# Kernel optimization log

Measured on AMD Instinct MI355X. Metric: run time of the kernel, lower is better.

## Reference

```python
import jax, jax.numpy as jnp
import numpy as np

SCALING = 32.0 / 16.0  # lora_alpha / r

HIDDEN = 4096
FFN = 14336
R = 16
TOKENS = 4096


def _lora(x, A, a_b, B, b_b):
    # nn.Linear: y = x @ W.T + b ; EVELinear: (B(A(x))) * scaling
    h = x @ A.T + a_b            # [tokens, r]
    return (h @ B.T + b_b) * SCALING  # [tokens, out]


def setup_inputs() -> dict:
    key = jax.random.key(0)
    ks = jax.random.split(key, 13)
    s = 0.02
    inp = {
        "x": jax.random.normal(ks[0], (TOKENS, HIDDEN), dtype=jnp.float32),
        # w1: hidden -> ffn
        "w1_A": jax.random.normal(ks[1], (R, HIDDEN), dtype=jnp.float32) * s,
        "w1_Ab": jax.random.normal(ks[2], (R,), dtype=jnp.float32) * s,
        "w1_B": jax.random.normal(ks[3], (FFN, R), dtype=jnp.float32) * s,
        "w1_Bb": jax.random.normal(ks[4], (FFN,), dtype=jnp.float32) * s,
        # w3: hidden -> ffn
        "w3_A": jax.random.normal(ks[5], (R, HIDDEN), dtype=jnp.float32) * s,
        "w3_Ab": jax.random.normal(ks[6], (R,), dtype=jnp.float32) * s,
        "w3_B": jax.random.normal(ks[7], (FFN, R), dtype=jnp.float32) * s,
        "w3_Bb": jax.random.normal(ks[8], (FFN,), dtype=jnp.float32) * s,
        # w2: ffn -> hidden
        "w2_A": jax.random.normal(ks[9], (R, FFN), dtype=jnp.float32) * s,
        "w2_Ab": jax.random.normal(ks[10], (R,), dtype=jnp.float32) * s,
        "w2_B": jax.random.normal(ks[11], (HIDDEN, R), dtype=jnp.float32) * s,
        "w2_Bb": jax.random.normal(ks[12], (HIDDEN,), dtype=jnp.float32) * s,
    }
    return inp


def reference(x, w1_A, w1_Ab, w1_B, w1_Bb, w3_A, w3_Ab, w3_B, w3_Bb,
              w2_A, w2_Ab, w2_B, w2_Bb):
    g = _lora(x, w1_A, w1_Ab, w1_B, w1_Bb)   # [tokens, ffn]
    u = _lora(x, w3_A, w3_Ab, w3_B, w3_Bb)   # [tokens, ffn]
    h = jax.nn.silu(g) * u                   # SwiGLU gate
    return _lora(h, w2_A, w2_Ab, w2_B, w2_Bb)  # [tokens, hidden]
```

## Files before the change

kernel.cpp:

```cpp
#include <hip/hip_runtime.h>

#define TOKENS 4096
#define HIDDEN 4096
#define FFN    14336
#define SCALING 2.0f

typedef short short8 __attribute__((ext_vector_type(8)));
typedef float f32x16 __attribute__((ext_vector_type(16)));

#define OFF_WAPK   ((size_t)0)
#define OFF_W1BPK  ((size_t)262144)
#define OFF_W3BPK  ((size_t)720896)
#define OFF_W2APK  ((size_t)1179648)
#define OFF_B1PK   ((size_t)2097152)
#define OFF_B3PK   ((size_t)2154496)
#define OFF_H13PK  ((size_t)2211840)
#define OFF_SLAB   ((size_t)2473984)
#define OFF_H2S    ((size_t)4571136)

__device__ __forceinline__ uint32_t pk_bf16(float a, float b) {
    uint32_t r;
    asm("v_cvt_pk_bf16_f32 %0, %1, %2" : "=v"(r) : "v"(a), "v"(b));
    return r;
}

__global__ __launch_bounds__(256) void p0_pack(
    const float* __restrict__ w1A, const float* __restrict__ w3A,
    const float* __restrict__ w1B, const float* __restrict__ w3B,
    const float* __restrict__ w2A,
    const float* __restrict__ w1Bb, const float* __restrict__ w3Bb,
    char* __restrict__ ws)
{
    const int g = blockIdx.x * 256 + threadIdx.x;

    if (g < 16384) {
        int l = g & 63, kt = g >> 6, c = l & 31, h = l >> 5;
        int k = kt * 16 + 8 * h;
        const float* s = (c < 16) ? (w1A + (size_t)c * HIDDEN + k)
                                  : (w3A + (size_t)(c - 16) * HIDDEN + k);
        float4 a = *(const float4*)s, b = *(const float4*)(s + 4);
        uint4 o = make_uint4(pk_bf16(a.x, a.y), pk_bf16(a.z, a.w),
                             pk_bf16(b.x, b.y), pk_bf16(b.z, b.w));
        ((uint4*)(ws + OFF_WAPK))[g] = o;
    } else if (g < 45056) {
        int t = g - 16384, l = t & 63, ft = t >> 6, c = l & 31, h = l >> 5;
        const float* s = w1B + (size_t)(ft * 32 + c) * 16 + 8 * h;
        float4 a = *(const float4*)s, b = *(const float4*)(s + 4);
        uint4 o = make_uint4(pk_bf16(a.x * 2.f, a.y * 2.f), pk_bf16(a.z * 2.f, a.w * 2.f),
                             pk_bf16(b.x * 2.f, b.y * 2.f), pk_bf16(b.z * 2.f, b.w * 2.f));
        ((uint4*)(ws + OFF_W1BPK))[t] = o;
    } else if (g < 73728) {
        int t = g - 45056, l = t & 63, ft = t >> 6, c = l & 31, h = l >> 5;
        const float* s = w3B + (size_t)(ft * 32 + c) * 16 + 8 * h;
        float4 a = *(const float4*)s, b = *(const float4*)(s + 4);
        uint4 o = make_uint4(pk_bf16(a.x * 2.f, a.y * 2.f), pk_bf16(a.z * 2.f, a.w * 2.f),
                             pk_bf16(b.x * 2.f, b.y * 2.f), pk_bf16(b.z * 2.f, b.w * 2.f));
        ((uint4*)(ws + OFF_W3BPK))[t] = o;
    } else if (g < 131072) {
        int t = g - 73728, l = t & 63, st = t >> 6, c = l & 31, h = l >> 5;
        uint4 o = make_uint4(0u, 0u, 0u, 0u);
        if (c < 16) {
            const float* s = w2A + (size_t)c * FFN + st * 16 + 8 * h;
            float4 a = *(const float4*)s, b = *(const float4*)(s + 4);
            o = make_uint4(pk_bf16(a.x, a.y), pk_bf16(a.z, a.w),
                           pk_bf16(b.x, b.y), pk_bf16(b.z, b.w));
        }
        ((uint4*)(ws + OFF_W2APK))[t] = o;
    } else if (g < 145408) {
        int t = g - 131072, ft = t >> 5, rest = t & 31, h = rest >> 4, j = rest & 15;
        int f = ft * 32 + (j & 3) + 8 * (j >> 2) + 4 * h;
        ((float*)(ws + OFF_B1PK))[t] = 2.f * w1Bb[f];
    } else if (g < 159744) {
        int t = g - 145408, ft = t >> 5, rest = t & 31, h = rest >> 4, j = rest & 15;
        int f = ft * 32 + (j & 3) + 8 * (j >> 2) + 4 * h;
        ((float*)(ws + OFF_B3PK))[t] = 2.f * w3Bb[f];
    }
}

__global__ __launch_bounds__(256, 2) void k1_xproj(
    const float* __restrict__ x, const uint4* __restrict__ wApk,
    float* __restrict__ slab)
{
    __shared__ float s_red[4][32][32];
    const int tid = threadIdx.x;
    const int w = tid >> 6, l = tid & 63, c = l & 31, h = l >> 5;
    const int t0 = blockIdx.x * 32;
    const int by = blockIdx.y;

    f32x16 acc;
    #pragma unroll
    for (int j = 0; j < 16; ++j) acc[j] = 0.f;

    const float* xr = x + (size_t)(t0 + c) * HIDDEN + 8 * h;
    const int kt0 = by * 64 + w * 16;
    #pragma unroll 4
    for (int kt = kt0; kt < kt0 + 16; ++kt) {
        const float* xp = xr + kt * 16;
        float4 a0 = *(const float4*)xp, a1 = *(const float4*)(xp + 4);
        uint4 ua = make_uint4(pk_bf16(a0.x, a0.y), pk_bf16(a0.z, a0.w),
                              pk_bf16(a1.x, a1.y), pk_bf16(a1.z, a1.w));
        short8 av = __builtin_bit_cast(short8, ua);
        short8 bv = __builtin_bit_cast(short8, wApk[(size_t)kt * 64 + l]);
        acc = __builtin_amdgcn_mfma_f32_32x32x16_bf16(av, bv, acc, 0, 0, 0);
    }
    #pragma unroll
    for (int j = 0; j < 16; ++j) {
        int row = (j & 3) + 8 * (j >> 2) + 4 * h;
        s_red[w][row][c] = acc[j];
    }
    __syncthreads();
    float* sl = slab + (size_t)by * TOKENS * 32;
    for (int p = tid; p < 1024; p += 256) {
        int row = p >> 5, cc = p & 31;
        float s = s_red[0][row][cc] + s_red[1][row][cc]
                + s_red[2][row][cc] + s_red[3][row][cc];
        sl[(size_t)(t0 + row) * 32 + cc] = s;
    }
}

__global__ __launch_bounds__(256) void k1b_combine(
    const float* __restrict__ slab,
    const float* __restrict__ w1Ab, const float* __restrict__ w3Ab,
    uint4* __restrict__ h13pk)
{
    const int g = blockIdx.x * 256 + threadIdx.x;
    const int l = g & 63, c = l & 31, h = l >> 5;
    const int tt = g >> 6;
    const int token = tt * 32 + c;

    float a[8], b[8];
    {
        float4 a0 = *(const float4*)(w1Ab + 8 * h), a1 = *(const float4*)(w1Ab + 8 * h + 4);
        float4 b0 = *(const float4*)(w3Ab + 8 * h), b1 = *(const float4*)(w3Ab + 8 * h + 4);
        a[0]=a0.x; a[1]=a0.y; a[2]=a0.z; a[3]=a0.w; a[4]=a1.x; a[5]=a1.y; a[6]=a1.z; a[7]=a1.w;
        b[0]=b0.x; b[1]=b0.y; b[2]=b0.z; b[3]=b0.w; b[4]=b1.x; b[5]=b1.y; b[6]=b1.z; b[7]=b1.w;
    }
    #pragma unroll
    for (int s = 0; s < 4; ++s) {
        const float* p = slab + ((size_t)s * TOKENS + token) * 32 + 8 * h;
        float4 v0 = *(const float4*)p,        v1 = *(const float4*)(p + 4);
        float4 u0 = *(const float4*)(p + 16), u1 = *(const float4*)(p + 20);
        a[0]+=v0.x; a[1]+=v0.y; a[2]+=v0.z; a[3]+=v0.w;
        a[4]+=v1.x; a[5]+=v1.y; a[6]+=v1.z; a[7]+=v1.w;
        b[0]+=u0.x; b[1]+=u0.y; b[2]+=u0.z; b[3]+=u0.w;
        b[4]+=u1.x; b[5]+=u1.y; b[6]+=u1.z; b[7]+=u1.w;
    }
    h13pk[(size_t)g * 2]     = make_uint4(pk_bf16(a[0],a[1]), pk_bf16(a[2],a[3]),
                                          pk_bf16(a[4],a[5]), pk_bf16(a[6],a[7]));
    h13pk[(size_t)g * 2 + 1] = make_uint4(pk_bf16(b[0],b[1]), pk_bf16(b[2],b[3]),
                                          pk_bf16(b[4],b[5]), pk_bf16(b[6],b[7]));
}

__global__ __launch_bounds__(256, 3) void k2_mid(
    const uint4* __restrict__ h13pk,
    const uint4* __restrict__ w1bpk, const uint4* __restrict__ w3bpk,
    const uint4* __restrict__ w2apk,
    const float* __restrict__ b1pk, const float* __restrict__ b3pk,
    float* __restrict__ h2s)
{
    __shared__ float s_acc[4][32][16];
    const int tid = threadIdx.x;
    const int w = tid >> 6, l = tid & 63, c = l & 31, h = l >> 5;
    const int tt = blockIdx.x, t0 = tt * 32, by = blockIdx.y;

    const short8 hA8 = __builtin_bit_cast(short8, h13pk[(size_t)(tt * 64 + l) * 2]);
    const short8 hB8 = __builtin_bit_cast(short8, h13pk[(size_t)(tt * 64 + l) * 2 + 1]);

    f32x16 acc;
    #pragma unroll
    for (int j = 0; j < 16; ++j) acc[j] = 0.f;

    #pragma unroll 2
    for (int it = 0; it < 16; ++it) {
        const int ft = by * 64 + w * 16 + it;
        short8 a1g = __builtin_bit_cast(short8, w1bpk[(size_t)ft * 64 + l]);
        short8 a1u = __builtin_bit_cast(short8, w3bpk[(size_t)ft * 64 + l]);
        short8 b2a = __builtin_bit_cast(short8, w2apk[(size_t)(ft * 2) * 64 + l]);
        short8 b2b = __builtin_bit_cast(short8, w2apk[(size_t)(ft * 2 + 1) * 64 + l]);

        const float* bg = b1pk + ((size_t)ft * 2 + h) * 16;
        const float* bu = b3pk + ((size_t)ft * 2 + h) * 16;
        float4 g0 = *(const float4*)bg,       g1 = *(const float4*)(bg + 4);
        float4 g2 = *(const float4*)(bg + 8), g3 = *(const float4*)(bg + 12);
        float4 u0 = *(const float4*)bu,       u1 = *(const float4*)(bu + 4);
        float4 u2 = *(const float4*)(bu + 8), u3 = *(const float4*)(bu + 12);
        f32x16 Cg, Cu;
        Cg[0]=g0.x; Cg[1]=g0.y; Cg[2]=g0.z; Cg[3]=g0.w;
        Cg[4]=g1.x; Cg[5]=g1.y; Cg[6]=g1.z; Cg[7]=g1.w;
        Cg[8]=g2.x; Cg[9]=g2.y; Cg[10]=g2.z; Cg[11]=g2.w;
        Cg[12]=g3.x; Cg[13]=g3.y; Cg[14]=g3.z; Cg[15]=g3.w;
        Cu[0]=u0.x; Cu[1]=u0.y; Cu[2]=u0.z; Cu[3]=u0.w;
        Cu[4]=u1.x; Cu[5]=u1.y; Cu[6]=u1.z; Cu[7]=u1.w;
        Cu[8]=u2.x; Cu[9]=u2.y; Cu[10]=u2.z; Cu[11]=u2.w;
        Cu[12]=u3.x; Cu[13]=u3.y; Cu[14]=u3.z; Cu[15]=u3.w;

        f32x16 d1g = __builtin_amdgcn_mfma_f32_32x32x16_bf16(a1g, hA8, Cg, 0, 0, 0);
        f32x16 d1u = __builtin_amdgcn_mfma_f32_32x32x16_bf16(a1u, hB8, Cu, 0, 0, 0);

        float hv[16];
        #pragma unroll
        for (int j = 0; j < 16; ++j) {
            float gg = d1g[j];
            float sig = __builtin_amdgcn_rcpf(1.f + __expf(-gg));
            hv[j] = gg * sig * d1u[j];
        }
        uint32_t q0 = pk_bf16(hv[0], hv[1]),   q1 = pk_bf16(hv[2], hv[3]);
        uint32_t q2 = pk_bf16(hv[4], hv[5]),   q3 = pk_bf16(hv[6], hv[7]);
        uint32_t q4 = pk_bf16(hv[8], hv[9]),   q5 = pk_bf16(hv[10], hv[11]);
        uint32_t q6 = pk_bf16(hv[12], hv[13]), q7 = pk_bf16(hv[14], hv[15]);
        asm("v_permlane32_swap_b32 %0, %1" : "+v"(q0), "+v"(q2));
        asm("v_permlane32_swap_b32 %0, %1" : "+v"(q1), "+v"(q3));
        asm("v_permlane32_swap_b32 %0, %1" : "+v"(q4), "+v"(q6));
        asm("v_permlane32_swap_b32 %0, %1" : "+v"(q5), "+v"(q7));
        short8 a2a = __builtin_bit_cast(short8, make_uint4(q0, q1, q2, q3));
        short8 a2b = __builtin_bit_cast(short8, make_uint4(q4, q5, q6, q7));

        acc = __builtin_amdgcn_mfma_f32_32x32x16_bf16(a2a, b2a, acc, 0, 0, 0);
        acc = __builtin_amdgcn_mfma_f32_32x32x16_bf16(a2b, b2b, acc, 0, 0, 0);
    }

    if (c < 16) {
        #pragma unroll
        for (int j = 0; j < 16; ++j)
            s_acc[w][(j & 3) + 8 * (j >> 2) + 4 * h][c] = acc[j];
    }
    __syncthreads();
    for (int p = tid; p < 512; p += 256) {
        int tok = p >> 4, r = p & 15;
        float s = s_acc[0][tok][r] + s_acc[1][tok][r] + s_acc[2][tok][r] + s_acc[3][tok][r];
        h2s[((size_t)by * TOKENS + t0 + tok) * 16 + r] = s;
    }
}

__global__ __launch_bounds__(256) void k3_out(
    const float* __restrict__ h2s,
    const float* __restrict__ w2Ab,
    const float* __restrict__ w2B, const float* __restrict__ w2Bb,
    float* __restrict__ out)
{
    __shared__ float s_h2[16][16];
    const int tid = threadIdx.x;
    const int t0 = blockIdx.x * 16;
    const int o0 = blockIdx.y * 1024;

    {
        int t = tid >> 4, r = tid & 15;
        float a = w2Ab[r];
        #pragma unroll
        for (int s = 0; s < 7; ++s)
            a += h2s[((size_t)s * TOKENS + t0 + t) * 16 + r];
        s_h2[t][r] = a;
    }
    __syncthreads();

    const int ob = o0 + tid * 4;
    float w[4][16];
    #pragma unroll
    for (int j = 0; j < 4; ++j) {
        #pragma unroll
        for (int k = 0; k < 4; ++k) {
            float4 v = *(const float4*)(w2B + (size_t)(ob + j) * 16 + k * 4);
            w[j][4*k+0] = v.x; w[j][4*k+1] = v.y;
            w[j][4*k+2] = v.z; w[j][4*k+3] = v.w;
        }
    }
    float4 bb = *(const float4*)(w2Bb + ob);
    float bias[4] = {bb.x, bb.y, bb.z, bb.w};

    for (int t = 0; t < 16; ++t) {
        float res[4];
        #pragma unroll
        for (int j = 0; j < 4; ++j) {
            float a = bias[j];
            #pragma unroll
            for (int r = 0; r < 16; ++r)
                a = fmaf(s_h2[t][r], w[j][r], a);
            res[j] = a * SCALING;
        }
        *(float4*)(out + (size_t)(t0 + t) * 4096 + ob) =
            make_float4(res[0], res[1], res[2], res[3]);
    }
}

extern "C" void kernel_launch(void* const* d_in, const int* in_sizes, int n_in,
                              void* d_out, int out_size, void* d_ws, size_t ws_size,
                              hipStream_t stream) {
    const float* x    = (const float*)d_in[0];
    const float* w1A  = (const float*)d_in[1];
    const float* w1Ab = (const float*)d_in[2];
    const float* w1B  = (const float*)d_in[3];
    const float* w1Bb = (const float*)d_in[4];
    const float* w3A  = (const float*)d_in[5];
    const float* w3Ab = (const float*)d_in[6];
    const float* w3B  = (const float*)d_in[7];
    const float* w3Bb = (const float*)d_in[8];
    const float* w2A  = (const float*)d_in[9];
    const float* w2Ab = (const float*)d_in[10];
    const float* w2B  = (const float*)d_in[11];
    const float* w2Bb = (const float*)d_in[12];
    float* out = (float*)d_out;

    char* ws = (char*)d_ws;
    const uint4* wApk  = (const uint4*)(ws + OFF_WAPK);
    const uint4* w1bpk = (const uint4*)(ws + OFF_W1BPK);
    const uint4* w3bpk = (const uint4*)(ws + OFF_W3BPK);
    const uint4* w2apk = (const uint4*)(ws + OFF_W2APK);
    const float* b1pk  = (const float*)(ws + OFF_B1PK);
    const float* b3pk  = (const float*)(ws + OFF_B3PK);
    uint4* h13pk = (uint4*)(ws + OFF_H13PK);
    float* slab  = (float*)(ws + OFF_SLAB);
    float* h2s   = (float*)(ws + OFF_H2S);

    p0_pack<<<624, 256, 0, stream>>>(w1A, w3A, w1B, w3B, w2A, w1Bb, w3Bb, ws);
    k1_xproj<<<dim3(128, 4), 256, 0, stream>>>(x, wApk, slab);
    k1b_combine<<<32, 256, 0, stream>>>(slab, w1Ab, w3Ab, h13pk);
    k2_mid<<<dim3(128, 7), 256, 0, stream>>>(h13pk, w1bpk, w3bpk, w2apk, b1pk, b3pk, h2s);
    k3_out<<<dim3(256, 4), 256, 0, stream>>>(h2s, w2Ab, w2B, w2Bb, out);
}
```

Baseline: 86.78 us.

## Fold A-weight packing into xproj and slab combine into mid kernel

Drops the separate bf16 packing of the w1/w3 A matrices and converts them on the fly inside k1_xproj. Removes the k1b_combine kernel by having each k2_mid block reduce the four split-K slabs and add the A biases itself, so one launch and the h13 round-trip go away. The bias loads in the mid kernel become a single vector load. The cost is that each of the 7 y-blocks repeats the slab reduction, and xproj now reads fp32 weights and spends extra conversion instructions.

```diff
diff --git a/kernel.cpp b/kernel.cpp
--- a/kernel.cpp
+++ b/kernel.cpp
@@ -8,15 +8,13 @@
 typedef short short8 __attribute__((ext_vector_type(8)));
 typedef float f32x16 __attribute__((ext_vector_type(16)));
 
-#define OFF_WAPK   ((size_t)0)
-#define OFF_W1BPK  ((size_t)262144)
-#define OFF_W3BPK  ((size_t)720896)
-#define OFF_W2APK  ((size_t)1179648)
-#define OFF_B1PK   ((size_t)2097152)
-#define OFF_B3PK   ((size_t)2154496)
-#define OFF_H13PK  ((size_t)2211840)
-#define OFF_SLAB   ((size_t)2473984)
-#define OFF_H2S    ((size_t)4571136)
+#define OFF_W1BPK  ((size_t)0)
+#define OFF_W3BPK  ((size_t)458752)
+#define OFF_W2APK  ((size_t)917504)
+#define OFF_B1PK   ((size_t)1835008)
+#define OFF_B3PK   ((size_t)1892352)
+#define OFF_SLAB   ((size_t)1949696)
+#define OFF_H2S    ((size_t)4046848)
 
 __device__ __forceinline__ uint32_t pk_bf16(float a, float b) {
     uint32_t r;
@@ -25,7 +23,6 @@
 }
 
 __global__ __launch_bounds__(256) void p0_pack(
-    const float* __restrict__ w1A, const float* __restrict__ w3A,
     const float* __restrict__ w1B, const float* __restrict__ w3B,
     const float* __restrict__ w2A,
     const float* __restrict__ w1Bb, const float* __restrict__ w3Bb,
@@ -33,31 +30,22 @@
 {
     const int g = blockIdx.x * 256 + threadIdx.x;
 
-    if (g < 16384) {
-        int l = g & 63, kt = g >> 6, c = l & 31, h = l >> 5;
-        int k = kt * 16 + 8 * h;
-        const float* s = (c < 16) ? (w1A + (size_t)c * HIDDEN + k)
-                                  : (w3A + (size_t)(c - 16) * HIDDEN + k);
-        float4 a = *(const float4*)s, b = *(const float4*)(s + 4);
-        uint4 o = make_uint4(pk_bf16(a.x, a.y), pk_bf16(a.z, a.w),
-                             pk_bf16(b.x, b.y), pk_bf16(b.z, b.w));
-        ((uint4*)(ws + OFF_WAPK))[g] = o;
-    } else if (g < 45056) {
-        int t = g - 16384, l = t & 63, ft = t >> 6, c = l & 31, h = l >> 5;
+    if (g < 28672) {
+        int l = g & 63, ft = g >> 6, c = l & 31, h = l >> 5;
         const float* s = w1B + (size_t)(ft * 32 + c) * 16 + 8 * h;
         float4 a = *(const float4*)s, b = *(const float4*)(s + 4);
         uint4 o = make_uint4(pk_bf16(a.x * 2.f, a.y * 2.f), pk_bf16(a.z * 2.f, a.w * 2.f),
                              pk_bf16(b.x * 2.f, b.y * 2.f), pk_bf16(b.z * 2.f, b.w * 2.f));
-        ((uint4*)(ws + OFF_W1BPK))[t] = o;
-    } else if (g < 73728) {
-        int t = g - 45056, l = t & 63, ft = t >> 6, c = l & 31, h = l >> 5;
+        ((uint4*)(ws + OFF_W1BPK))[g] = o;
+    } else if (g < 57344) {
+        int t = g - 28672, l = t & 63, ft = t >> 6, c = l & 31, h = l >> 5;
         const float* s = w3B + (size_t)(ft * 32 + c) * 16 + 8 * h;
         float4 a = *(const float4*)s, b = *(const float4*)(s + 4);
         uint4 o = make_uint4(pk_bf16(a.x * 2.f, a.y * 2.f), pk_bf16(a.z * 2.f, a.w * 2.f),
                              pk_bf16(b.x * 2.f, b.y * 2.f), pk_bf16(b.z * 2.f, b.w * 2.f));
         ((uint4*)(ws + OFF_W3BPK))[t] = o;
-    } else if (g < 131072) {
-        int t = g - 73728, l = t & 63, st = t >> 6, c = l & 31, h = l >> 5;
+    } else if (g < 114688) {
+        int t = g - 57344, l = t & 63, st = t >> 6, c = l & 31, h = l >> 5;
         uint4 o = make_uint4(0u, 0u, 0u, 0u);
         if (c < 16) {
             const float* s = w2A + (size_t)c * FFN + st * 16 + 8 * h;
@@ -66,19 +54,20 @@
                            pk_bf16(b.x, b.y), pk_bf16(b.z, b.w));
         }
         ((uint4*)(ws + OFF_W2APK))[t] = o;
-    } else if (g < 145408) {
-        int t = g - 131072, ft = t >> 5, rest = t & 31, h = rest >> 4, j = rest & 15;
+    } else if (g < 129024) {
+        int t = g - 114688, ft = t >> 5, rest = t & 31, h = rest >> 4, j = rest & 15;
         int f = ft * 32 + (j & 3) + 8 * (j >> 2) + 4 * h;
         ((float*)(ws + OFF_B1PK))[t] = 2.f * w1Bb[f];
-    } else if (g < 159744) {
-        int t = g - 145408, ft = t >> 5, rest = t & 31, h = rest >> 4, j = rest & 15;
+    } else if (g < 143360) {
+        int t = g - 129024, ft = t >> 5, rest = t & 31, h = rest >> 4, j = rest & 15;
         int f = ft * 32 + (j & 3) + 8 * (j >> 2) + 4 * h;
         ((float*)(ws + OFF_B3PK))[t] = 2.f * w3Bb[f];
     }
 }
 
 __global__ __launch_bounds__(256, 2) void k1_xproj(
-    const float* __restrict__ x, const uint4* __restrict__ wApk,
+    const float* __restrict__ x,
+    const float* __restrict__ w1A, const float* __restrict__ w3A,
     float* __restrict__ slab)
 {
     __shared__ float s_red[4][32][32];
@@ -92,15 +81,21 @@
     for (int j = 0; j < 16; ++j) acc[j] = 0.f;
 
     const float* xr = x + (size_t)(t0 + c) * HIDDEN + 8 * h;
+    const float* wr = ((c < 16) ? (w1A + (size_t)c * HIDDEN)
+                                : (w3A + (size_t)(c - 16) * HIDDEN)) + 8 * h;
     const int kt0 = by * 64 + w * 16;
     #pragma unroll 4
     for (int kt = kt0; kt < kt0 + 16; ++kt) {
-        const float* xp = xr + kt * 16;
+        const float* xp = xr + (size_t)kt * 16;
+        const float* wp = wr + (size_t)kt * 16;
         float4 a0 = *(const float4*)xp, a1 = *(const float4*)(xp + 4);
-        uint4 ua = make_uint4(pk_bf16(a0.x, a0.y), pk_bf16(a0.z, a0.w),
-                              pk_bf16(a1.x, a1.y), pk_bf16(a1.z, a1.w));
-        short8 av = __builtin_bit_cast(short8, ua);
-        short8 bv = __builtin_bit_cast(short8, wApk[(size_t)kt * 64 + l]);
+        float4 b0 = *(const float4*)wp, b1 = *(const float4*)(wp + 4);
+        short8 av = __builtin_bit_cast(short8,
+            make_uint4(pk_bf16(a0.x, a0.y), pk_bf16(a0.z, a0.w),
+                       pk_bf16(a1.x, a1.y), pk_bf16(a1.z, a1.w)));
+        short8 bv = __builtin_bit_cast(short8,
+            make_uint4(pk_bf16(b0.x, b0.y), pk_bf16(b0.z, b0.w),
+                       pk_bf16(b1.x, b1.y), pk_bf16(b1.z, b1.w)));
         acc = __builtin_amdgcn_mfma_f32_32x32x16_bf16(av, bv, acc, 0, 0, 0);
     }
     #pragma unroll
@@ -118,15 +113,18 @@
     }
 }
 
-__global__ __launch_bounds__(256) void k1b_combine(
+__global__ __launch_bounds__(256, 3) void k2_mid(
     const float* __restrict__ slab,
     const float* __restrict__ w1Ab, const float* __restrict__ w3Ab,
-    uint4* __restrict__ h13pk)
-{
-    const int g = blockIdx.x * 256 + threadIdx.x;
-    const int l = g & 63, c = l & 31, h = l >> 5;
-    const int tt = g >> 6;
-    const int token = tt * 32 + c;
+    const uint4* __restrict__ w1bpk, const uint4* __restrict__ w3bpk,
+    const uint4* __restrict__ w2apk,
+    const float* __restrict__ b1pk, const float* __restrict__ b3pk,
+    float* __restrict__ h2s)
+{
+    __shared__ float s_acc[4][32][16];
+    const int tid = threadIdx.x;
+    const int w = tid >> 6, l = tid & 63, c = l & 31, h = l >> 5;
+    const int tt = blockIdx.x, t0 = tt * 32, by = blockIdx.y;
 
     float a[8], b[8];
     {
@@ -137,7 +135,7 @@
     }
     #pragma unroll
     for (int s = 0; s < 4; ++s) {
-        const float* p = slab + ((size_t)s * TOKENS + token) * 32 + 8 * h;
+        const float* p = slab + ((size_t)s * TOKENS + t0 + c) * 32 + 8 * h;
         float4 v0 = *(const float4*)p,        v1 = *(const float4*)(p + 4);
         float4 u0 = *(const float4*)(p + 16), u1 = *(const float4*)(p + 20);
         a[0]+=v0.x; a[1]+=v0.y; a[2]+=v0.z; a[3]+=v0.w;
@@ -145,26 +143,12 @@
         b[0]+=u0.x; b[1]+=u0.y; b[2]+=u0.z; b[3]+=u0.w;
         b[4]+=u1.x; b[5]+=u1.y; b[6]+=u1.z; b[7]+=u1.w;
     }
-    h13pk[(size_t)g * 2]     = make_uint4(pk_bf16(a[0],a[1]), pk_bf16(a[2],a[3]),
-                                          pk_bf16(a[4],a[5]), pk_bf16(a[6],a[7]));
-    h13pk[(size_t)g * 2 + 1] = make_uint4(pk_bf16(b[0],b[1]), pk_bf16(b[2],b[3]),
-                                          pk_bf16(b[4],b[5]), pk_bf16(b[6],b[7]));
-}
-
-__global__ __launch_bounds__(256, 3) void k2_mid(
-    const uint4* __restrict__ h13pk,
-    const uint4* __restrict__ w1bpk, const uint4* __restrict__ w3bpk,
-    const uint4* __restrict__ w2apk,
-    const float* __restrict__ b1pk, const float* __restrict__ b3pk,
-    float* __restrict__ h2s)
-{
-    __shared__ float s_acc[4][32][16];
-    const int tid = threadIdx.x;
-    const int w = tid >> 6, l = tid & 63, c = l & 31, h = l >> 5;
-    const int tt = blockIdx.x, t0 = tt * 32, by = blockIdx.y;
-
-    const short8 hA8 = __builtin_bit_cast(short8, h13pk[(size_t)(tt * 64 + l) * 2]);
-    const short8 hB8 = __builtin_bit_cast(short8, h13pk[(size_t)(tt * 64 + l) * 2 + 1]);
+    const short8 hA8 = __builtin_bit_cast(short8,
+        make_uint4(pk_bf16(a[0],a[1]), pk_bf16(a[2],a[3]),
+                   pk_bf16(a[4],a[5]), pk_bf16(a[6],a[7])));
+    const short8 hB8 = __builtin_bit_cast(short8,
+        make_uint4(pk_bf16(b[0],b[1]), pk_bf16(b[2],b[3]),
+                   pk_bf16(b[4],b[5]), pk_bf16(b[6],b[7])));
 
     f32x16 acc;
     #pragma unroll
@@ -178,21 +162,8 @@
         short8 b2a = __builtin_bit_cast(short8, w2apk[(size_t)(ft * 2) * 64 + l]);
         short8 b2b = __builtin_bit_cast(short8, w2apk[(size_t)(ft * 2 + 1) * 64 + l]);
 
-        const float* bg = b1pk + ((size_t)ft * 2 + h) * 16;
-        const float* bu = b3pk + ((size_t)ft * 2 + h) * 16;
-        float4 g0 = *(const float4*)bg,       g1 = *(const float4*)(bg + 4);
-        float4 g2 = *(const float4*)(bg + 8), g3 = *(const float4*)(bg + 12);
-        float4 u0 = *(const float4*)bu,       u1 = *(const float4*)(bu + 4);
-        float4 u2 = *(const float4*)(bu + 8), u3 = *(const float4*)(bu + 12);
-        f32x16 Cg, Cu;
-        Cg[0]=g0.x; Cg[1]=g0.y; Cg[2]=g0.z; Cg[3]=g0.w;
-        Cg[4]=g1.x; Cg[5]=g1.y; Cg[6]=g1.z; Cg[7]=g1.w;
-        Cg[8]=g2.x; Cg[9]=g2.y; Cg[10]=g2.z; Cg[11]=g2.w;
-        Cg[12]=g3.x; Cg[13]=g3.y; Cg[14]=g3.z; Cg[15]=g3.w;
-        Cu[0]=u0.x; Cu[1]=u0.y; Cu[2]=u0.z; Cu[3]=u0.w;
-        Cu[4]=u1.x; Cu[5]=u1.y; Cu[6]=u1.z; Cu[7]=u1.w;
-        Cu[8]=u2.x; Cu[9]=u2.y; Cu[10]=u2.z; Cu[11]=u2.w;
-        Cu[12]=u3.x; Cu[13]=u3.y; Cu[14]=u3.z; Cu[15]=u3.w;
+        f32x16 Cg = *reinterpret_cast<const f32x16*>(b1pk + ((size_t)ft * 2 + h) * 16);
+        f32x16 Cu = *reinterpret_cast<const f32x16*>(b3pk + ((size_t)ft * 2 + h) * 16);
 
         f32x16 d1g = __builtin_amdgcn_mfma_f32_32x32x16_bf16(a1g, hA8, Cg, 0, 0, 0);
         f32x16 d1u = __builtin_amdgcn_mfma_f32_32x32x16_bf16(a1u, hB8, Cu, 0, 0, 0);
@@ -301,19 +272,17 @@
     float* out = (float*)d_out;
 
     char* ws = (char*)d_ws;
-    const uint4* wApk  = (const uint4*)(ws + OFF_WAPK);
     const uint4* w1bpk = (const uint4*)(ws + OFF_W1BPK);
     const uint4* w3bpk = (const uint4*)(ws + OFF_W3BPK);
     const uint4* w2apk = (const uint4*)(ws + OFF_W2APK);
     const float* b1pk  = (const float*)(ws + OFF_B1PK);
     const float* b3pk  = (const float*)(ws + OFF_B3PK);
-    uint4* h13pk = (uint4*)(ws + OFF_H13PK);
     float* slab  = (float*)(ws + OFF_SLAB);
     float* h2s   = (float*)(ws + OFF_H2S);
 
-    p0_pack<<<624, 256, 0, stream>>>(w1A, w3A, w1B, w3B, w2A, w1Bb, w3Bb, ws);
-    k1_xproj<<<dim3(128, 4), 256, 0, stream>>>(x, wApk, slab);
-    k1b_combine<<<32, 256, 0, stream>>>(slab, w1Ab, w3Ab, h13pk);
-    k2_mid<<<dim3(128, 7), 256, 0, stream>>>(h13pk, w1bpk, w3bpk, w2apk, b1pk, b3pk, h2s);
+    p0_pack<<<560, 256, 0, stream>>>(w1B, w3B, w2A, w1Bb, w3Bb, ws);
+    k1_xproj<<<dim3(128, 4), 256, 0, stream>>>(x, w1A, w3A, slab);
+    k2_mid<<<dim3(128, 7), 256, 0, stream>>>(slab, w1Ab, w3Ab,
+                                             w1bpk, w3bpk, w2apk, b1pk, b3pk, h2s);
     k3_out<<<dim3(256, 4), 256, 0, stream>>>(h2s, w2Ab, w2B, w2Bb, out);
 }
```

New measurement: 94.40 us. 1.09x slower.
